# Kernel optimization log

Measured on AMD Instinct MI355X. Metric: run time of the kernel, lower is better.

Reference implementation:

```python
import jax, jax.numpy as jnp
import numpy as np

P = 50000      # number of graph nodes (cortical dipoles)
HID = 256      # hidden width
E = 800000     # number of nonzeros in Ahat (avg degree 16)


def setup_inputs() -> dict:
    key = jax.random.key(0)
    ks = jax.random.split(key, 12)
    beta = jax.random.normal(ks[0], (P, 1), dtype=jnp.float32)
    degree = jax.random.uniform(ks[1], (P, 1), dtype=jnp.float32)
    A_rows = jax.random.randint(ks[2], (E,), 0, P, dtype=jnp.int32)
    A_cols = jax.random.randint(ks[3], (E,), 0, P, dtype=jnp.int32)
    # normalized-adjacency-like positive values
    A_vals = jax.random.uniform(ks[4], (E,), dtype=jnp.float32) * (1.0 / 16.0)
    # parameters (torch nn.Linear stores weight as [out, in])
    s_in = 1.0 / np.sqrt(3.0)
    s_h = 1.0 / np.sqrt(HID)
    W_in = jax.random.uniform(ks[5], (HID, 3), jnp.float32, -s_in, s_in)
    b_in = jax.random.uniform(ks[6], (HID,), jnp.float32, -s_in, s_in)
    W_mp1 = jax.random.uniform(ks[7], (HID, HID), jnp.float32, -s_h, s_h)
    W_mp2 = jax.random.uniform(ks[8], (HID, HID), jnp.float32, -s_h, s_h)
    W_out = jax.random.uniform(ks[9], (1, HID), jnp.float32, -s_h, s_h)
    b_out = jax.random.uniform(ks[10], (1,), jnp.float32, -s_h, s_h)
    return {
        "beta": beta, "degree": degree,
        "A_rows": A_rows, "A_cols": A_cols, "A_vals": A_vals,
        "W_in": W_in, "b_in": b_in,
        "W_mp1": W_mp1, "W_mp2": W_mp2,
        "W_out": W_out, "b_out": b_out,
    }


def _spmm(A_rows, A_cols, A_vals, X):
    # sparse [P,P] @ dense [P,H] via gather + segment-sum over COO edges
    msgs = A_vals[:, None] * X[A_cols]            # [E, H]
    return jax.ops.segment_sum(msgs, A_rows, num_segments=P)


def reference(beta, degree, A_rows, A_cols, A_vals,
              W_in, b_in, W_mp1, W_mp2, W_out, b_out):
    x = jnp.concatenate([beta, beta ** 2, degree], axis=1)   # [P, 3]
    h = jax.nn.relu(x @ W_in.T + b_in)                       # [P, HID]
    AH = _spmm(A_rows, A_cols, A_vals, h)                    # one-hop
    A2H = _spmm(A_rows, A_cols, A_vals, AH)                  # two-hop
    h = jax.nn.relu(AH @ W_mp1.T + A2H @ W_mp2.T)            # fused sum + relu
    g = jax.nn.softplus(h @ W_out.T + b_out)                 # [P, 1]
    return g
```

## Files before the change

kernel.cpp:

```cpp
#include <hip/hip_runtime.h>
#include <math.h>

#define NP 50000
#define HIDDEN 256
#define NE 800000
#define CAP 64

#define OFF_AH     0ULL
#define OFF_A2H    25600000ULL
#define OFF_BP     51200000ULL
#define OFF_CNT    51462144ULL
#define OFF_PC     51662144ULL
#define OFF_EV     52062144ULL

typedef __attribute__((ext_vector_type(8))) short bf16x8;
typedef __attribute__((ext_vector_type(8))) unsigned short u16x8;
typedef __attribute__((ext_vector_type(4))) float f32x4;

__device__ inline unsigned short f2bf(float f) {
    union { float f; unsigned int u; } x; x.f = f;
    unsigned int r = x.u + 0x7FFFu + ((x.u >> 16) & 1u);
    return (unsigned short)(r >> 16);
}
__device__ inline float bf2f(unsigned short u) {
    union { unsigned int u; float f; } x; x.u = ((unsigned int)u) << 16; return x.f;
}

__global__ void bp_kernel(const float* __restrict__ W1,
                          const float* __restrict__ W2,
                          unsigned short* __restrict__ Bp) {
    int t = blockIdx.x * 256 + threadIdx.x;
    int j = t >> 9;
    int k = t & 511;
    float v = (k < 256) ? W1[j * 256 + k] : W2[j * 256 + (k - 256)];
    Bp[(k >> 3) * 2048 + j * 8 + (k & 7)] = f2bf(v);
}

__global__ void pc_kernel(const float* __restrict__ beta,
                          const float* __restrict__ degree,
                          float2* __restrict__ pc) {
    int i = blockIdx.x * 256 + threadIdx.x;
    if (i < NP) pc[i] = make_float2(beta[i], degree[i]);
}

__global__ void scatter_ell(const int* __restrict__ rows,
                            const int* __restrict__ cols,
                            const float* __restrict__ vals,
                            int* __restrict__ cnt,
                            int2* __restrict__ ev) {
    int e = blockIdx.x * 256 + threadIdx.x;
    if (e < NE) {
        int r = rows[e];
        int pos = atomicAdd(&cnt[r], 1);
        if (pos < CAP)
            ev[(size_t)r * CAP + pos] = make_int2(cols[e], __float_as_int(vals[e]));
    }
}

__global__ __launch_bounds__(256) void spmm_embed_kernel(
        const int* __restrict__ cnt, const int2* __restrict__ ev,
        const float2* __restrict__ pc,
        const float* __restrict__ W_in, const float* __restrict__ b_in,
        unsigned short* __restrict__ Y) {
    int w = threadIdx.x >> 6;
    int lane = threadIdx.x & 63;
    int r = blockIdx.x * 4 + w;
    if (r >= NP) return;
    int half = lane >> 5;
    int fo = (lane & 31) * 8;

    int n = min(cnt[r], CAP);
    int2 e2 = make_int2(0, 0);
    if (lane < n) e2 = ev[(size_t)r * CAP + lane];
    int col_l = e2.x;
    float val_l = __int_as_float(e2.y);

    float wr0[8], wr1[8], wr2[8], br[8];
    #pragma unroll
    for (int j = 0; j < 8; ++j) {
        wr0[j] = W_in[(fo + j) * 3 + 0];
        wr1[j] = W_in[(fo + j) * 3 + 1];
        wr2[j] = W_in[(fo + j) * 3 + 2];
        br[j]  = b_in[fo + j];
    }

    float acc[8] = {0.f,0.f,0.f,0.f,0.f,0.f,0.f,0.f};

#define ESTEP(d)                                                             \
    {                                                                        \
        float2 pr[d]; float vr[d];                                           \
        _Pragma("unroll")                                                    \
        for (int k = 0; k < (d); ++k) {                                      \
            int e = i + 2 * k + half;                                        \
            int c = __shfl(col_l, e);                                        \
            vr[k] = __shfl(val_l, e);                                        \
            pr[k] = pc[c];                                                   \
        }                                                                    \
        _Pragma("unroll")                                                    \
        for (int k = 0; k < (d); ++k) {                                      \
            float b = pr[k].x, dd = pr[k].y, v = vr[k];                      \
            float b2 = b * b;                                                \
            _Pragma("unroll")                                                \
            for (int j = 0; j < 8; ++j) {                                    \
                float t = fmaf(b, wr0[j], fmaf(b2, wr1[j], fmaf(dd, wr2[j], br[j]))); \
                acc[j] = fmaf(v, fmaxf(t, 0.f), acc[j]);                     \
            }                                                                \
        }                                                                    \
    }

    int i = 0;
    for (; i + 16 <= n; i += 16) ESTEP(8)
    if (i + 8 <= n) { ESTEP(4) i += 8; }
    if (i + 4 <= n) { ESTEP(2) i += 4; }
    if (i < n)      { ESTEP(2) }
#undef ESTEP

    #pragma unroll
    for (int j = 0; j < 8; ++j) acc[j] += __shfl_xor(acc[j], 32);
    if (half == 0) {
        u16x8 o;
        #pragma unroll
        for (int j = 0; j < 8; ++j) o[j] = f2bf(acc[j]);
        *reinterpret_cast<u16x8*>(Y + (size_t)r * HIDDEN + fo) = o;
    }
}

__global__ __launch_bounds__(256) void spmm_gather_kernel(
        const int* __restrict__ cnt, const int2* __restrict__ ev,
        const unsigned short* __restrict__ X,
        unsigned short* __restrict__ Y) {
    int w = threadIdx.x >> 6;
    int lane = threadIdx.x & 63;
    int r = blockIdx.x * 4 + w;
    if (r >= NP) return;
    int half = lane >> 5;
    int fo = (lane & 31) * 8;

    int n = min(cnt[r], CAP);
    int2 e2 = make_int2(0, 0);
    if (lane < n) e2 = ev[(size_t)r * CAP + lane];
    int col_l = e2.x;
    float val_l = __int_as_float(e2.y);

    float acc[8] = {0.f,0.f,0.f,0.f,0.f,0.f,0.f,0.f};

#define GSTEP(d)                                                             \
    {                                                                        \
        u16x8 xr[d]; float vr[d];                                            \
        _Pragma("unroll")                                                    \
        for (int k = 0; k < (d); ++k) {                                      \
            int e = i + 2 * k + half;                                        \
            int c = __shfl(col_l, e);                                        \
            vr[k] = __shfl(val_l, e);                                        \
            xr[k] = *reinterpret_cast<const u16x8*>(X + (size_t)c * HIDDEN + fo); \
        }                                                                    \
        _Pragma("unroll")                                                    \
        for (int k = 0; k < (d); ++k)                                        \
            _Pragma("unroll")                                                \
            for (int j = 0; j < 8; ++j)                                      \
                acc[j] = fmaf(vr[k], bf2f(xr[k][j]), acc[j]);                \
    }

    int i = 0;
    for (; i + 16 <= n; i += 16) GSTEP(8)
    if (i + 8 <= n) { GSTEP(4) i += 8; }
    if (i + 4 <= n) { GSTEP(2) i += 4; }
    if (i < n)      { GSTEP(2) }
#undef GSTEP

    #pragma unroll
    for (int j = 0; j < 8; ++j) acc[j] += __shfl_xor(acc[j], 32);
    if (half == 0) {
        u16x8 o;
        #pragma unroll
        for (int j = 0; j < 8; ++j) o[j] = f2bf(acc[j]);
        *reinterpret_cast<u16x8*>(Y + (size_t)r * HIDDEN + fo) = o;
    }
}

__global__ __launch_bounds__(512, 4) void mp_out_kernel(
        const unsigned short* __restrict__ AH,
        const unsigned short* __restrict__ A2H,
        const unsigned short* __restrict__ Bp,
        const float* __restrict__ W_out, const float* __restrict__ b_out,
        float* __restrict__ g) {
    __shared__ unsigned short As[128 * 64];
    __shared__ unsigned short Bs[8 * 256 * 8];
    __shared__ float Ps[4][128];

    int tid = threadIdx.x;
    int w = tid >> 6;
    int lane = tid & 63;
    int wr = w >> 2;
    int wc = w & 3;
    int p0 = blockIdx.x * 128;

    f32x4 acc[4][4];
    #pragma unroll
    for (int i = 0; i < 4; ++i)
        #pragma unroll
        for (int j = 0; j < 4; ++j)
            acc[i][j] = (f32x4){0.f, 0.f, 0.f, 0.f};

    for (int kc = 0; kc < 8; ++kc) {
        const unsigned short* Xsrc = (kc < 4) ? AH : A2H;
        int k0 = (kc & 3) * 64;
        __syncthreads();
        #pragma unroll
        for (int it = 0; it < 2; ++it) {
            int slot = it * 512 + tid;
            int ss = slot ^ ((slot >> 3) & 7);
            int row = ss >> 3;
            int ko = (ss & 7) * 8;
            int grow = p0 + row;
            if (grow >= NP) grow = NP - 1;
            float4 v = *reinterpret_cast<const float4*>(Xsrc + (size_t)grow * HIDDEN + k0 + ko);
            *reinterpret_cast<float4*>(&As[slot * 8]) = v;
        }
        #pragma unroll
        for (int it = 0; it < 4; ++it) {
            int c2 = it * 512 + tid;
            float4 v = *reinterpret_cast<const float4*>(
                Bp + ((size_t)(kc * 8 + (c2 >> 8))) * 2048 + (c2 & 255) * 8);
            *reinterpret_cast<float4*>(&Bs[c2 * 8]) = v;
        }
        __syncthreads();
        #pragma unroll
        for (int ks = 0; ks < 2; ++ks) {
            bf16x8 af[4], bfr[4];
            #pragma unroll
            for (int rt = 0; rt < 4; ++rt) {
                int row = wr * 64 + rt * 16 + (lane & 15);
                int elem = row * 64 + ks * 32 + (lane >> 4) * 8;
                elem ^= (row & 7) << 3;
                af[rt] = *reinterpret_cast<const bf16x8*>(&As[elem]);
            }
            #pragma unroll
            for (int nt = 0; nt < 4; ++nt) {
                int col = wc * 64 + nt * 16 + (lane & 15);
                int kbl = ks * 4 + (lane >> 4);
                bfr[nt] = *reinterpret_cast<const bf16x8*>(&Bs[kbl * 2048 + col * 8]);
            }
            #pragma unroll
            for (int rt = 0; rt < 4; ++rt)
                #pragma unroll
                for (int nt = 0; nt < 4; ++nt)
                    acc[rt][nt] = __builtin_amdgcn_mfma_f32_16x16x32_bf16(
                        af[rt], bfr[nt], acc[rt][nt], 0, 0, 0);
        }
    }

    float wv[4];
    #pragma unroll
    for (int nt = 0; nt < 4; ++nt)
        wv[nt] = W_out[wc * 64 + nt * 16 + (lane & 15)];

    float ps[4][4];
    #pragma unroll
    for (int rt = 0; rt < 4; ++rt)
        #pragma unroll
        for (int r = 0; r < 4; ++r) {
            float s = 0.f;
            #pragma unroll
            for (int nt = 0; nt < 4; ++nt)
                s = fmaf(fmaxf(acc[rt][nt][r], 0.0f), wv[nt], s);
            ps[rt][r] = s;
        }
    #pragma unroll
    for (int m = 1; m < 16; m <<= 1)
        #pragma unroll
        for (int rt = 0; rt < 4; ++rt)
            #pragma unroll
            for (int r = 0; r < 4; ++r)
                ps[rt][r] += __shfl_xor(ps[rt][r], m);

    if ((lane & 15) == 0) {
        int rb = wr * 64 + (lane >> 4) * 4;
        #pragma unroll
        for (int rt = 0; rt < 4; ++rt)
            #pragma unroll
            for (int r = 0; r < 4; ++r)
                Ps[wc][rb + rt * 16 + r] = ps[rt][r];
    }
    __syncthreads();
    if (tid < 128) {
        int p = p0 + tid;
        if (p < NP) {
            float z = Ps[0][tid] + Ps[1][tid] + Ps[2][tid] + Ps[3][tid] + b_out[0];
            g[p] = fmaxf(z, 0.0f) + log1pf(expf(-fabsf(z)));
        }
    }
}

extern "C" void kernel_launch(void* const* d_in, const int* in_sizes, int n_in,
                              void* d_out, int out_size, void* d_ws, size_t ws_size,
                              hipStream_t stream) {
    const float* beta   = (const float*)d_in[0];
    const float* degree = (const float*)d_in[1];
    const int*   A_rows = (const int*)d_in[2];
    const int*   A_cols = (const int*)d_in[3];
    const float* A_vals = (const float*)d_in[4];
    const float* W_in   = (const float*)d_in[5];
    const float* b_in   = (const float*)d_in[6];
    const float* W_mp1  = (const float*)d_in[7];
    const float* W_mp2  = (const float*)d_in[8];
    const float* W_out  = (const float*)d_in[9];
    const float* b_out  = (const float*)d_in[10];
    float* g = (float*)d_out;

    char* ws = (char*)d_ws;
    unsigned short* AH  = (unsigned short*)(ws + OFF_AH);
    unsigned short* A2H = (unsigned short*)(ws + OFF_A2H);
    unsigned short* Bp  = (unsigned short*)(ws + OFF_BP);
    int*    cnt = (int*)(ws + OFF_CNT);
    float2* pc  = (float2*)(ws + OFF_PC);
    int2*   ev  = (int2*)(ws + OFF_EV);

    hipMemsetAsync(cnt, 0, NP * sizeof(int), stream);

    bp_kernel<<<512, 256, 0, stream>>>(W_mp1, W_mp2, Bp);
    pc_kernel<<<(NP + 255) / 256, 256, 0, stream>>>(beta, degree, pc);

    scatter_ell<<<(NE + 255) / 256, 256, 0, stream>>>(A_rows, A_cols, A_vals, cnt, ev);

    spmm_embed_kernel<<<(NP + 3) / 4, 256, 0, stream>>>(cnt, ev, pc, W_in, b_in, AH);
    spmm_gather_kernel<<<(NP + 3) / 4, 256, 0, stream>>>(cnt, ev, AH, A2H);

    mp_out_kernel<<<(NP + 127) / 128, 512, 0, stream>>>(AH, A2H, Bp, W_out, b_out, g);
}
```

Baseline: 175.2 us.

## Split hidden features into two planes and gather each half in separate passes

```diff
diff --git a/kernel.cpp b/kernel.cpp
--- a/kernel.cpp
+++ b/kernel.cpp
@@ -12,6 +12,8 @@
 #define OFF_CNT    51462144ULL
 #define OFF_PC     51662144ULL
 #define OFF_EV     52062144ULL
+
+#define HPLANE (NP * 128)
 
 typedef __attribute__((ext_vector_type(8))) short bf16x8;
 typedef __attribute__((ext_vector_type(8))) unsigned short u16x8;
@@ -121,11 +123,13 @@
         u16x8 o;
         #pragma unroll
         for (int j = 0; j < 8; ++j) o[j] = f2bf(acc[j]);
-        *reinterpret_cast<u16x8*>(Y + (size_t)r * HIDDEN + fo) = o;
-    }
-}
-
-__global__ __launch_bounds__(256) void spmm_gather_kernel(
+        int f = fo >> 7;
+        int off = fo & 127;
+        *reinterpret_cast<u16x8*>(Y + (size_t)f * HPLANE + (size_t)r * 128 + off) = o;
+    }
+}
+
+__global__ __launch_bounds__(256) void spmm_gather_half(
         const int* __restrict__ cnt, const int2* __restrict__ ev,
         const unsigned short* __restrict__ X,
         unsigned short* __restrict__ Y) {
@@ -133,8 +137,8 @@
     int lane = threadIdx.x & 63;
     int r = blockIdx.x * 4 + w;
     if (r >= NP) return;
-    int half = lane >> 5;
-    int fo = (lane & 31) * 8;
+    int q = lane >> 4;
+    int fo = (lane & 15) * 8;
 
     int n = min(cnt[r], CAP);
     int2 e2 = make_int2(0, 0);
@@ -144,15 +148,18 @@
 
     float acc[8] = {0.f,0.f,0.f,0.f,0.f,0.f,0.f,0.f};
 
-#define GSTEP(d)                                                             \
+#define GS(d, MASKED)                                                        \
     {                                                                        \
         u16x8 xr[d]; float vr[d];                                            \
         _Pragma("unroll")                                                    \
         for (int k = 0; k < (d); ++k) {                                      \
-            int e = i + 2 * k + half;                                        \
-            int c = __shfl(col_l, e);                                        \
-            vr[k] = __shfl(val_l, e);                                        \
-            xr[k] = *reinterpret_cast<const u16x8*>(X + (size_t)c * HIDDEN + fo); \
+            int e = i + 4 * k + q;                                           \
+            int es = (MASKED) ? (e & 63) : e;                                \
+            int c = __shfl(col_l, es);                                       \
+            float vt = __shfl(val_l, es);                                    \
+            if (MASKED) vt = (e < n) ? vt : 0.f;                             \
+            vr[k] = vt;                                                      \
+            xr[k] = *reinterpret_cast<const u16x8*>(X + (size_t)c * 128 + fo); \
         }                                                                    \
         _Pragma("unroll")                                                    \
         for (int k = 0; k < (d); ++k)                                        \
@@ -162,19 +169,22 @@
     }
 
     int i = 0;
-    for (; i + 16 <= n; i += 16) GSTEP(8)
-    if (i + 8 <= n) { GSTEP(4) i += 8; }
-    if (i + 4 <= n) { GSTEP(2) i += 4; }
-    if (i < n)      { GSTEP(2) }
-#undef GSTEP
-
-    #pragma unroll
-    for (int j = 0; j < 8; ++j) acc[j] += __shfl_xor(acc[j], 32);
-    if (half == 0) {
+    for (; i + 32 <= n; i += 32) GS(8, false)
+    if (i + 16 <= n) { GS(4, false) i += 16; }
+    if (i + 8 <= n)  { GS(2, false) i += 8; }
+    if (i < n)       { GS(2, true) }
+#undef GS
+
+    #pragma unroll
+    for (int j = 0; j < 8; ++j) {
+        acc[j] += __shfl_xor(acc[j], 16);
+        acc[j] += __shfl_xor(acc[j], 32);
+    }
+    if (q == 0) {
         u16x8 o;
         #pragma unroll
         for (int j = 0; j < 8; ++j) o[j] = f2bf(acc[j]);
-        *reinterpret_cast<u16x8*>(Y + (size_t)r * HIDDEN + fo) = o;
+        *reinterpret_cast<u16x8*>(Y + (size_t)r * 128 + fo) = o;
     }
 }
 
@@ -203,8 +213,10 @@
             acc[i][j] = (f32x4){0.f, 0.f, 0.f, 0.f};
 
     for (int kc = 0; kc < 8; ++kc) {
-        const unsigned short* Xsrc = (kc < 4) ? AH : A2H;
-        int k0 = (kc & 3) * 64;
+        const unsigned short* Xb = (kc < 4) ? AH : A2H;
+        int kcl = kc & 3;
+        const unsigned short* Xsrc = Xb + (size_t)(kcl >> 1) * HPLANE;
+        int k0h = (kcl & 1) * 64;
         __syncthreads();
         #pragma unroll
         for (int it = 0; it < 2; ++it) {
@@ -214,7 +226,7 @@
             int ko = (ss & 7) * 8;
             int grow = p0 + row;
             if (grow >= NP) grow = NP - 1;
-            float4 v = *reinterpret_cast<const float4*>(Xsrc + (size_t)grow * HIDDEN + k0 + ko);
+            float4 v = *reinterpret_cast<const float4*>(Xsrc + (size_t)grow * 128 + k0h + ko);
             *reinterpret_cast<float4*>(&As[slot * 8]) = v;
         }
         #pragma unroll
@@ -324,7 +336,9 @@
     scatter_ell<<<(NE + 255) / 256, 256, 0, stream>>>(A_rows, A_cols, A_vals, cnt, ev);
 
     spmm_embed_kernel<<<(NP + 3) / 4, 256, 0, stream>>>(cnt, ev, pc, W_in, b_in, AH);
-    spmm_gather_kernel<<<(NP + 3) / 4, 256, 0, stream>>>(cnt, ev, AH, A2H);
+
+    spmm_gather_half<<<(NP + 3) / 4, 256, 0, stream>>>(cnt, ev, AH, A2H);
+    spmm_gather_half<<<(NP + 3) / 4, 256, 0, stream>>>(cnt, ev, AH + HPLANE, A2H + HPLANE);
 
     mp_out_kernel<<<(NP + 127) / 128, 512, 0, stream>>>(AH, A2H, Bp, W_out, b_out, g);
 }
```

New measurement: 186.3 us. 6.3% more time.
